# Performance work log

Measured on AMD Instinct MI355X. Metric: run time of the kernel, lower is better.

The kernel has to match this reference:

```python
import jax, jax.numpy as jnp
import numpy as np
from jax import lax

EPS = 1e-5

def _conv(x, w, pad):
    # x: NCHW, w: OIHW, stride 1
    return lax.conv_general_dilated(x, w, (1, 1), [(pad, pad), (pad, pad)],
                                    dimension_numbers=('NCHW', 'OIHW', 'NCHW'))

def _binconv(x, w):
    # IR-Net/ReActNet HardBinaryConv: sign-binarized weights scaled by per-filter
    # mean |w| (alpha), sign-binarized activations; clip-based STE for backward.
    alpha = jnp.mean(jnp.abs(w), axis=(1, 2, 3), keepdims=True)  # [O,1,1,1]
    wc = jnp.clip(w, -1.0, 1.0)
    bw = lax.stop_gradient(alpha * jnp.sign(w) - wc) + wc
    xc = jnp.clip(x, -1.0, 1.0)
    ba = lax.stop_gradient(jnp.sign(x) - xc) + xc
    return _conv(ba, bw, 1)

def _bn(x, g, b, m, v):
    # inference-mode BatchNorm2d with running stats
    inv = g / jnp.sqrt(v + EPS)
    return x * inv[None, :, None, None] + (b - m * inv)[None, :, None, None]

def _pool(x):
    return lax.reduce_window(x, -jnp.inf, lax.max, (1, 1, 2, 2), (1, 1, 2, 2), 'VALID')

def _htanh(x):
    return jnp.clip(x, -1.0, 1.0)

def setup_inputs() -> dict:
    key = jax.random.key(0)
    ks = jax.random.split(key, 40)
    B = 256
    d = {'x': jax.random.normal(ks[0], (B, 3, 32, 32), jnp.float32)}
    shapes = [(128, 3, 3, 3), (128, 128, 3, 3), (256, 128, 3, 3),
              (256, 256, 3, 3), (512, 256, 3, 3), (512, 512, 3, 3)]
    chans = [128, 128, 256, 256, 512, 512]
    ki = 1
    for i, (ws, c) in enumerate(zip(shapes, chans)):
        fan_in = ws[1] * 9
        d[f'w{i}'] = jax.random.normal(ks[ki], ws, jnp.float32) / np.sqrt(fan_in); ki += 1
        d[f'g{i}'] = jnp.ones((c,), jnp.float32)
        d[f'b{i}'] = jnp.zeros((c,), jnp.float32)
        d[f'm{i}'] = jax.random.normal(ks[ki], (c,), jnp.float32) * 0.1; ki += 1
        d[f'v{i}'] = jax.random.uniform(ks[ki], (c,), jnp.float32, 0.5, 1.5); ki += 1
    d['fcw'] = jax.random.normal(ks[ki], (10, 512 * 4 * 4), jnp.float32) * 0.01
    d['fcb'] = jnp.zeros((10,), jnp.float32)
    return d

def reference(x, w0, g0, b0, m0, v0, w1, g1, b1, m1, v1, w2, g2, b2, m2, v2,
              w3, g3, b3, m3, v3, w4, g4, b4, m4, v4, w5, g5, b5, m5, v5,
              fcw, fcb):
    h = _bn(_conv(x, w0, 1), g0, b0, m0, v0)            # [B,128,32,32]
    h = _htanh(_bn(_pool(_binconv(h, w1)), g1, b1, m1, v1))   # [B,128,16,16]
    h = _htanh(_bn(_binconv(h, w2), g2, b2, m2, v2))          # [B,256,16,16]
    h = _htanh(_bn(_pool(_binconv(h, w3)), g3, b3, m3, v3))   # [B,256,8,8]
    h = _htanh(_bn(_binconv(h, w4), g4, b4, m4, v4))          # [B,512,8,8]
    h = _htanh(_bn(_pool(_binconv(h, w5)), g5, b5, m5, v5))   # [B,512,4,4]
    h = h.reshape(h.shape[0], -1)                             # [B,8192]
    return h @ fcw.T + fcb                                    # [B,10]
```

## Files before the change

### kernel.cpp

```cpp
#include <hip/hip_runtime.h>
#include <cstdint>

#define EPS 1e-5
typedef unsigned long long u64;
typedef unsigned int u32;
typedef unsigned short u16;

struct BnArgs { const float *g[6], *b[6], *m[6], *v[6]; };
struct PackArgs { const float* w[5]; u64* wbt[5]; };

__global__ void bn_prep_all(BnArgs p, double* __restrict__ scale_all,
                            double* __restrict__ shift_all) {
    int i = blockIdx.x * 256 + threadIdx.x;
    if (i >= 1792) return;
    int l, base;
    if (i < 128)       { l = 0; base = 0; }
    else if (i < 256)  { l = 1; base = 128; }
    else if (i < 512)  { l = 2; base = 256; }
    else if (i < 768)  { l = 3; base = 512; }
    else if (i < 1280) { l = 4; base = 768; }
    else               { l = 5; base = 1280; }
    const int c = i - base;
    double inv = (double)p.g[l][c] / sqrt((double)p.v[l][c] + EPS);
    scale_all[i] = inv;
    shift_all[i] = (double)p.b[l][c] - (double)p.m[l][c] * inv;
}

__global__ void zero_out(float* __restrict__ out, int n) {
    int i = blockIdx.x * blockDim.x + threadIdx.x;
    if (i < n) out[i] = 0.f;
}

__global__ void zero_u64(u64* __restrict__ p, size_t n) {
    size_t i = (size_t)blockIdx.x * 256 + threadIdx.x;
    const size_t step = (size_t)gridDim.x * 256;
    for (; i < n; i += step) p[i] = 0ull;
}

__global__ void pack_all(PackArgs pk, const double* __restrict__ scale_all,
                         const double* __restrict__ shift_all,
                         double* __restrict__ A_all,
                         int* __restrict__ tlt_all, int* __restrict__ tgt_all,
                         u32* __restrict__ ct_all) {
    const int ob = blockIdx.x;
    const int t = threadIdx.x;
    int l, base, Cin, bnoff, OTOT, ctoff;
    if (ob < 128)       { l = 0; base = 0;    Cin = 128; bnoff = 128;  OTOT = 128; ctoff = 0; }
    else if (ob < 384)  { l = 1; base = 128;  Cin = 128; bnoff = 256;  OTOT = 256; ctoff = 2048; }
    else if (ob < 640)  { l = 2; base = 384;  Cin = 256; bnoff = 512;  OTOT = 256; ctoff = 6144; }
    else if (ob < 1152) { l = 3; base = 640;  Cin = 256; bnoff = 768;  OTOT = 512; ctoff = 10240; }
    else                { l = 4; base = 1152; Cin = 512; bnoff = 1280; OTOT = 512; ctoff = 18432; }
    const int o = ob - base;
    const float* wo = pk.w[l] + (size_t)o * Cin * 9;

    double s = 0.0;
    for (int k = t; k < Cin * 9; k += 256) s += fabs((double)wo[k]);
    __shared__ double red[256];
    __shared__ u32 stp[9];
    red[t] = s;
    if (t < 9) stp[t] = 0;
    __syncthreads();
    for (int r = 128; r > 0; r >>= 1) {
        if (t < r) red[t] += red[t + r];
        __syncthreads();
    }
    if (t == 0) {
        double alpha = red[0] / (double)(Cin * 9);
        const double dA = alpha * scale_all[bnoff + o];
        const double dB = shift_all[bnoff + o];
        A_all[ob] = dA;
        const int INF = 1 << 30;
        int Tlt, Tgt = INF;
        if (dA > 0.0) {
            const double tt = -dB / dA;
            if (!(fabs(tt) < 6000.0)) {
                Tlt = (dB < 0.0) ? INF : -INF;
            } else {
                int v0 = (int)floor(tt) - 4;
                int c = INF;
                for (int v = v0; v < v0 + 9; ++v)
                    if (fma(dA, (double)v, dB) >= 0.0) { c = v; break; }
                Tlt = c;
            }
        } else if (dA < 0.0) {
            const double tt = -dB / dA;
            if (!(fabs(tt) < 6000.0)) {
                Tlt = (dB < 0.0) ? INF : -INF;
            } else {
                int v0 = (int)floor(tt) - 4;
                int c = INF;
                for (int v = v0; v < v0 + 9; ++v)
                    if (fma(dA, (double)v, dB) < 0.0) { c = v; break; }
                Tlt = -INF;
                Tgt = (c == INF) ? INF : (c - 1);
            }
        } else {
            Tlt = (dB < 0.0) ? INF : -INF;
        }
        tlt_all[ob] = Tlt;
        tgt_all[ob] = Tgt;
    }

    const int W64 = Cin / 64;
    u64* wbt = pk.wbt[l];
    for (int e = t; e < 9 * W64; e += 256) {
        int tap = e / W64, word = e % W64;
        u64 bits = 0;
        for (int j = 0; j < 64; ++j) {
            int c = word * 64 + j;
            if (wo[c * 9 + tap] < 0.f) bits |= (1ull << j);
        }
        wbt[((size_t)tap * OTOT + o) * W64 + word] = bits;
        atomicAdd(&stp[tap], (u32)__popcll(bits));
    }
    __syncthreads();

    if (t < 16) {
        const int pat = t;
        int nv = 0;
        u32 cor = 0;
#pragma unroll
        for (int tap = 0; tap < 9; ++tap) {
            const int dy = tap / 3, dx = tap % 3;
            const bool inv = ((pat & 1) && dy == 0) || ((pat & 2) && dy == 2) ||
                             ((pat & 4) && dx == 0) || ((pat & 8) && dx == 2);
            if (inv) cor += stp[tap]; else nv++;
        }
        ct_all[ctoff + pat * OTOT + o] = (u32)(nv * 64 * W64) + 2u * cor;
    }
}

__global__ __launch_bounds__(256) void conv0_pack(
        const float* __restrict__ x, const float* __restrict__ w0,
        const double* __restrict__ scale, const double* __restrict__ shift,
        u64* __restrict__ bits0) {
    __shared__ double wlds[128 * 27];
    __shared__ double sc[128], sh[128];
    const int tid = threadIdx.x;
    for (int e = tid; e < 128 * 27; e += 256) wlds[e] = (double)w0[e];
    for (int e = tid; e < 128; e += 256) { sc[e] = scale[e]; sh[e] = shift[e]; }
    __syncthreads();

    const int n = blockIdx.y;
    const int p = blockIdx.x * 256 + tid;
    const int y = p >> 5, xx = p & 31;
    const float* xn = x + (size_t)n * 3 * 32 * 32;

    double win[27];
#pragma unroll
    for (int c = 0; c < 3; ++c)
#pragma unroll
        for (int dy = 0; dy < 3; ++dy)
#pragma unroll
            for (int dx = 0; dx < 3; ++dx) {
                const int yy = y + dy - 1, xs = xx + dx - 1;
                const bool ok = (yy >= 0 && yy < 32 && xs >= 0 && xs < 32);
                win[(c * 3 + dy) * 3 + dx] = ok ? (double)xn[(c * 32 + yy) * 32 + xs] : 0.0;
            }

    u64* op = bits0 + (((size_t)n * 34 + (y + 1)) * 34 + (xx + 1)) * 2;
#pragma unroll
    for (int og = 0; og < 2; ++og) {
        u64 word = 0;
#pragma unroll 2
        for (int j = 0; j < 64; ++j) {
            const int o = og * 64 + j;
            const double* wo = &wlds[o * 27];
            double acc = 0.0;
#pragma unroll
            for (int k = 0; k < 27; ++k) acc = fma(wo[k], win[k], acc);
            const double val = acc * sc[o] + sh[o];
            word |= (u64)(val < 0.0) << j;
        }
        op[og] = word;
    }
}

template<int H, int W, int W64, int OTOT, int OPW, bool POOL, bool LAST, int MINW>
__global__ __launch_bounds__(256, MINW) void bconv7(
        const u64* __restrict__ in_bits, const u64* __restrict__ wbt,
        const double* __restrict__ A, const double* __restrict__ B,
        const int* __restrict__ tlt, const int* __restrict__ tgt,
        const u32* __restrict__ ct_all, int ctoff,
        u32* __restrict__ out_bits, float* __restrict__ h5) {
    const int tid = threadIdx.x;
    const int wave = tid >> 6, lane = tid & 63;
    constexpr int WPI = (H * W) / 64;
    const int img = (WPI >= 4) ? blockIdx.z : (blockIdx.z * 4 + wave);
    const int wii = (WPI >= 4) ? (blockIdx.y * 4 + wave) : 0;
    const int y = wii * (64 / W) + lane / W;
    const int x = lane % W;
    const int obase = blockIdx.x * OPW;

    __shared__ u32 ctl[16 * (OPW + 1)];
    for (int e = tid; e < 16 * OPW; e += 256) {
        const int pat = e / OPW, oc = e % OPW;
        ctl[pat * (OPW + 1) + oc] = ct_all[ctoff + pat * OTOT + obase + oc];
    }
    __syncthreads();

    constexpr int RC = W + 2;
    const u64* ib = in_bits + (size_t)img * (H + 2) * RC * W64;

    int acc[OPW];
#pragma unroll
    for (int oc = 0; oc < OPW; ++oc) acc[oc] = 0;

#pragma unroll 1
    for (int dy = 0; dy < 3; ++dy) {
#pragma unroll 1
        for (int dx = 0; dx < 3; ++dx) {
            const u64* q = ib + ((size_t)(y + dy) * RC + (x + dx)) * W64;
            u64 wn[W64];
#pragma unroll
            for (int k = 0; k < W64; ++k) wn[k] = q[k];
            const u64* wt = wbt + (size_t)((dy * 3 + dx) * OTOT + obase) * W64;
#pragma unroll
            for (int oc = 0; oc < OPW; ++oc) {
#pragma unroll
                for (int k = 0; k < W64; ++k)
                    acc[oc] += (int)__popcll(wn[k] ^ wt[oc * W64 + k]);
            }
        }
    }

    const int pat = (y == 0 ? 1 : 0) | (y == H - 1 ? 2 : 0) |
                    (x == 0 ? 4 : 0) | (x == W - 1 ? 8 : 0);
    const int ctbase = pat * (OPW + 1);
    constexpr int Hp = POOL ? H / 2 : H, Wp = POOL ? W / 2 : W;
    const bool writer = (!POOL) || (((lane & 1) == 0) && ((lane & W) == 0));
    const int py = POOL ? (y >> 1) : y, px = POOL ? (x >> 1) : x;

    u32 cur = 0;
#pragma unroll
    for (int oc = 0; oc < OPW; ++oc) {
        int v = (int)ctl[ctbase + oc] - 2 * acc[oc];
        if (POOL) {
            int v2 = max(v, __shfl_xor(v, 1, 64));
            v = max(v2, __shfl_xor(v2, W, 64));
        }
        if (LAST) {
            const double t = fma(A[obase + oc], (double)v, B[obase + oc]);
            const double hcl = fmin(1.0, fmax(-1.0, t));
            if (writer)
                h5[(((size_t)img * OTOT + obase + oc) * Hp + py) * Wp + px] = (float)hcl;
        } else {
            const bool bit = (v < tlt[obase + oc]) | (v > tgt[obase + oc]);
            cur |= (u32)bit << oc;
        }
    }
    if (!LAST && writer) {
        const size_t wordIdx =
            (((size_t)img * (Hp + 2) + (py + 1)) * (Wp + 2) + (px + 1)) * (OTOT / 32)
            + (obase >> 5);
        if (OPW == 32) {
            out_bits[wordIdx] = cur;
        } else {
            u16* o16 = (u16*)out_bits;
            o16[wordIdx * 2 + ((obase >> 4) & 1)] = (u16)cur;
        }
    }
}

__global__ void fc_kernel(const float* __restrict__ h, const float* __restrict__ fcw,
                          const float* __restrict__ fcb, float* __restrict__ out) {
    const int n = blockIdx.x, t = threadIdx.x;
    double acc[10];
#pragma unroll
    for (int j = 0; j < 10; ++j) acc[j] = 0.0;
    const float* hn = h + (size_t)n * 8192;
    for (int k = t; k < 8192; k += 256) {
        double xv = (double)hn[k];
#pragma unroll
        for (int j = 0; j < 10; ++j) acc[j] += xv * (double)fcw[j * 8192 + k];
    }
    __shared__ double red[10][256];
#pragma unroll
    for (int j = 0; j < 10; ++j) red[j][t] = acc[j];
    __syncthreads();
    for (int r = 128; r > 0; r >>= 1) {
        if (t < r) {
#pragma unroll
            for (int j = 0; j < 10; ++j) red[j][t] += red[j][t + r];
        }
        __syncthreads();
    }
    if (t < 10) out[n * 10 + t] = (float)(red[t][0] + (double)fcb[t]);
}

extern "C" void kernel_launch(void* const* d_in, const int* in_sizes, int n_in,
                              void* d_out, int out_size, void* d_ws, size_t ws_size,
                              hipStream_t stream) {
    const float* X = (const float*)d_in[0];
    BnArgs bn;
    PackArgs pk;
    const float* Wt0 = (const float*)d_in[1];
    for (int i = 0; i < 6; ++i) {
        bn.g[i] = (const float*)d_in[2 + 5 * i];
        bn.b[i] = (const float*)d_in[3 + 5 * i];
        bn.m[i] = (const float*)d_in[4 + 5 * i];
        bn.v[i] = (const float*)d_in[5 + 5 * i];
    }
    for (int i = 0; i < 5; ++i) pk.w[i] = (const float*)d_in[1 + 5 * (i + 1)];
    const float* fcw = (const float*)d_in[31];
    const float* fcb = (const float*)d_in[32];
    float* out = (float*)d_out;

    char* ws = (char*)d_ws;
    size_t off = 0;
    auto alloc = [&](size_t bytes) -> void* {
        void* p = ws + off;
        off = (off + bytes + 255) & ~(size_t)255;
        return p;
    };

    double* scale_all = (double*)alloc(1792 * sizeof(double));
    double* shift_all = (double*)alloc(1792 * sizeof(double));
    double* A_all     = (double*)alloc(1664 * sizeof(double));
    int* tlt_all      = (int*)alloc(1664 * sizeof(int));
    int* tgt_all      = (int*)alloc(1664 * sizeof(int));
    u32* ct_all       = (u32*)alloc(26624 * sizeof(u32));
    const size_t WBN[5] = {128ull * 9 * 2, 256ull * 9 * 2, 256ull * 9 * 4,
                           512ull * 9 * 4, 512ull * 9 * 8};
    for (int i = 0; i < 5; ++i) pk.wbt[i] = (u64*)alloc(WBN[i] * sizeof(u64));
    u64* bits4 = (u64*)alloc(256ull * 10 * 10 * 8 * sizeof(u64));
    u64* bits0 = (u64*)alloc(256ull * 34 * 34 * 2 * sizeof(u64));
    u64* bits1 = (u64*)alloc(256ull * 18 * 18 * 2 * sizeof(u64));
    u64* bits2 = (u64*)alloc(256ull * 18 * 18 * 4 * sizeof(u64));
    u64* bits3 = (u64*)alloc(256ull * 10 * 10 * 4 * sizeof(u64));
    const size_t bits_u64 =
        256ull * (10 * 10 * 8 + 34 * 34 * 2 + 18 * 18 * 2 + 18 * 18 * 4 + 10 * 10 * 4);
    float* h5 = (float*)bits0;
    {
        const size_t h5_bytes = 256ull * 8192 * sizeof(float);
        const size_t have = (size_t)((char*)(bits3 + 256ull * 10 * 10 * 4) - (char*)bits0);
        if (h5_bytes > have) alloc(h5_bytes - have);
    }

    if (off > ws_size) {
        zero_out<<<dim3((out_size + 255) / 256), dim3(256), 0, stream>>>(out, out_size);
        return;
    }

    const int BOF[6] = {0, 128, 256, 512, 768, 1280};
    const int AOF[5] = {0, 128, 384, 640, 1152};
    const int CTO[5] = {0, 2048, 6144, 10240, 18432};

    bn_prep_all<<<dim3(7), dim3(256), 0, stream>>>(bn, scale_all, shift_all);
    pack_all<<<dim3(1664), dim3(256), 0, stream>>>(pk, scale_all, shift_all,
                                                   A_all, tlt_all, tgt_all, ct_all);
    zero_u64<<<dim3(2048), dim3(256), 0, stream>>>(bits4, bits_u64);

    conv0_pack<<<dim3(4, 256), dim3(256), 0, stream>>>(
        X, Wt0, scale_all + BOF[0], shift_all + BOF[0], bits0);

    bconv7<32, 32, 2, 128, 32, true, false, 4><<<dim3(4, 4, 256), dim3(256), 0, stream>>>(
        bits0, pk.wbt[0], nullptr, nullptr, tlt_all + AOF[0], tgt_all + AOF[0],
        ct_all, CTO[0], (u32*)bits1, nullptr);
    bconv7<16, 16, 2, 256, 32, false, false, 4><<<dim3(8, 1, 256), dim3(256), 0, stream>>>(
        bits1, pk.wbt[1], nullptr, nullptr, tlt_all + AOF[1], tgt_all + AOF[1],
        ct_all, CTO[1], (u32*)bits2, nullptr);
    bconv7<16, 16, 4, 256, 32, true, false, 4><<<dim3(8, 1, 256), dim3(256), 0, stream>>>(
        bits2, pk.wbt[2], nullptr, nullptr, tlt_all + AOF[2], tgt_all + AOF[2],
        ct_all, CTO[2], (u32*)bits3, nullptr);
    bconv7<8, 8, 4, 512, 16, false, false, 8><<<dim3(32, 1, 64), dim3(256), 0, stream>>>(
        bits3, pk.wbt[3], nullptr, nullptr, tlt_all + AOF[3], tgt_all + AOF[3],
        ct_all, CTO[3], (u32*)bits4, nullptr);
    bconv7<8, 8, 8, 512, 16, true, true, 8><<<dim3(32, 1, 64), dim3(256), 0, stream>>>(
        bits4, pk.wbt[4], A_all + AOF[4], shift_all + BOF[5], nullptr, nullptr,
        ct_all, CTO[4], nullptr, h5);

    fc_kernel<<<dim3(256), dim3(256), 0, stream>>>(h5, fcw, fcb, out);
}
```

Before: 557.7 us.

## Run last binary conv on int8 MFMA instead of XNOR-popcount kernel

```diff
diff --git a/kernel.cpp b/kernel.cpp
--- a/kernel.cpp
+++ b/kernel.cpp
@@ -5,6 +5,7 @@
 typedef unsigned long long u64;
 typedef unsigned int u32;
 typedef unsigned short u16;
+typedef int v4i __attribute__((ext_vector_type(4)));
 
 struct BnArgs { const float *g[6], *b[6], *m[6], *v[6]; };
 struct PackArgs { const float* w[5]; u64* wbt[5]; };
@@ -41,7 +42,7 @@
                          const double* __restrict__ shift_all,
                          double* __restrict__ A_all,
                          int* __restrict__ tlt_all, int* __restrict__ tgt_all,
-                         u32* __restrict__ ct_all) {
+                         u32* __restrict__ ct_all, signed char* __restrict__ wi8) {
     const int ob = blockIdx.x;
     const int t = threadIdx.x;
     int l, base, Cin, bnoff, OTOT, ctoff;
@@ -113,6 +114,13 @@
         wbt[((size_t)tap * OTOT + o) * W64 + word] = bits;
         atomicAdd(&stp[tap], (u32)__popcll(bits));
     }
+    if (l == 4) {
+        for (int e = t; e < 9 * 512; e += 256) {
+            const int tap = e / 512, c = e % 512;
+            wi8[((size_t)tap * 512 + o) * 512 + c] =
+                (wo[c * 9 + tap] < 0.f) ? (signed char)-1 : (signed char)1;
+        }
+    }
     __syncthreads();
 
     if (t < 16) {
@@ -262,6 +270,95 @@
     }
 }
 
+__global__ __launch_bounds__(256, 2) void bconv5_mfma(
+        const u64* __restrict__ bits4, const signed char* __restrict__ wi8,
+        const double* __restrict__ A, const double* __restrict__ B,
+        float* __restrict__ h5) {
+    const int tid = threadIdx.x;
+    const int wave = tid >> 6, lane = tid & 63;
+    const int img = blockIdx.y;
+    const int nhalf = blockIdx.x;
+
+    __shared__ __align__(16) signed char act[100 * 528];
+    {
+        u32* a32 = (u32*)act;
+        for (int e = tid; e < 100 * 132; e += 256) a32[e] = 0;
+        __syncthreads();
+        for (int e = tid; e < 64 * 128; e += 256) {
+            const int px = e >> 7, wi = e & 127;
+            const int cell = (px >> 3) * 10 + (px & 7) + 11;
+            const u64 bb = bits4[((size_t)img * 100 + cell) * 8 + (wi >> 4)];
+            const u32 nib = (u32)(bb >> ((wi & 15) * 4)) & 0xF;
+            const u32 spread = (nib & 1) | ((nib & 2) << 7) |
+                               ((nib & 4) << 14) | ((nib & 8) << 21);
+            a32[cell * 132 + wi] = 0x01010101u + 254u * spread;
+        }
+    }
+    __syncthreads();
+
+    const int r16 = lane & 15, kg4 = lane >> 4;
+    const int ntb = nhalf * 16 + wave * 4;
+
+    v4i acc[4][4];
+#pragma unroll
+    for (int m = 0; m < 4; ++m)
+#pragma unroll
+        for (int q = 0; q < 4; ++q) acc[m][q] = (v4i){0, 0, 0, 0};
+
+    int acell[4];
+#pragma unroll
+    for (int m = 0; m < 4; ++m) {
+        const int px = m * 16 + r16;
+        acell[m] = ((px >> 3) + (m * 2 - (px >> 3) ? 0 : 0)) * 10 + (px & 7);
+        acell[m] = (m * 2 + (r16 >> 3)) * 10 + (r16 & 7);
+    }
+
+#pragma unroll 1
+    for (int tap = 0; tap < 9; ++tap) {
+        const int coff = (tap / 3) * 10 + (tap % 3);
+        const signed char* wb = wi8 + (size_t)tap * 512 * 512;
+#pragma unroll 1
+        for (int kg = 0; kg < 8; ++kg) {
+            const int kofs = kg * 64 + kg4 * 16;
+            v4i af[4];
+#pragma unroll
+            for (int m = 0; m < 4; ++m)
+                af[m] = *(const v4i*)&act[(acell[m] + coff) * 528 + kofs];
+#pragma unroll
+            for (int q = 0; q < 4; ++q) {
+                const int oc = (ntb + q) * 16 + r16;
+                const v4i bf = *(const v4i*)&wb[(size_t)oc * 512 + kofs];
+#pragma unroll
+                for (int m = 0; m < 4; ++m)
+                    acc[m][q] = __builtin_amdgcn_mfma_i32_16x16x64_i8(
+                        af[m], bf, acc[m][q], 0, 0, 0);
+            }
+        }
+    }
+
+#pragma unroll
+    for (int m = 0; m < 4; ++m) {
+#pragma unroll
+        for (int q = 0; q < 4; ++q) {
+            const int v01 = max(acc[m][q][0], acc[m][q][1]);
+            const int v23 = max(acc[m][q][2], acc[m][q][3]);
+            const int p0 = max(v01, __shfl_xor(v01, 32, 64));
+            const int p1 = max(v23, __shfl_xor(v23, 32, 64));
+            if (kg4 < 2) {
+                const int oc = (ntb + q) * 16 + r16;
+                const int py = m;
+                const int px0 = kg4 * 2;
+                const double Av = A[oc], Bv = B[oc];
+                const double t0 = fma(Av, (double)p0, Bv);
+                const double t1 = fma(Av, (double)p1, Bv);
+                float* hp = &h5[(((size_t)img * 512 + oc) * 4 + py) * 4 + px0];
+                hp[0] = (float)fmin(1.0, fmax(-1.0, t0));
+                hp[1] = (float)fmin(1.0, fmax(-1.0, t1));
+            }
+        }
+    }
+}
+
 __global__ void fc_kernel(const float* __restrict__ h, const float* __restrict__ fcw,
                           const float* __restrict__ fcb, float* __restrict__ out) {
     const int n = blockIdx.x, t = threadIdx.x;
@@ -320,6 +417,7 @@
     int* tlt_all      = (int*)alloc(1664 * sizeof(int));
     int* tgt_all      = (int*)alloc(1664 * sizeof(int));
     u32* ct_all       = (u32*)alloc(26624 * sizeof(u32));
+    signed char* wi8  = (signed char*)alloc(9ull * 512 * 512);
     const size_t WBN[5] = {128ull * 9 * 2, 256ull * 9 * 2, 256ull * 9 * 4,
                            512ull * 9 * 4, 512ull * 9 * 8};
     for (int i = 0; i < 5; ++i) pk.wbt[i] = (u64*)alloc(WBN[i] * sizeof(u64));
@@ -348,7 +446,7 @@
 
     bn_prep_all<<<dim3(7), dim3(256), 0, stream>>>(bn, scale_all, shift_all);
     pack_all<<<dim3(1664), dim3(256), 0, stream>>>(pk, scale_all, shift_all,
-                                                   A_all, tlt_all, tgt_all, ct_all);
+                                                   A_all, tlt_all, tgt_all, ct_all, wi8);
     zero_u64<<<dim3(2048), dim3(256), 0, stream>>>(bits4, bits_u64);
 
     conv0_pack<<<dim3(4, 256), dim3(256), 0, stream>>>(
@@ -366,9 +464,9 @@
     bconv7<8, 8, 4, 512, 16, false, false, 8><<<dim3(32, 1, 64), dim3(256), 0, stream>>>(
         bits3, pk.wbt[3], nullptr, nullptr, tlt_all + AOF[3], tgt_all + AOF[3],
         ct_all, CTO[3], (u32*)bits4, nullptr);
-    bconv7<8, 8, 8, 512, 16, true, true, 8><<<dim3(32, 1, 64), dim3(256), 0, stream>>>(
-        bits4, pk.wbt[4], A_all + AOF[4], shift_all + BOF[5], nullptr, nullptr,
-        ct_all, CTO[4], nullptr, h5);
+
+    bconv5_mfma<<<dim3(2, 256), dim3(256), 0, stream>>>(
+        bits4, wi8, A_all + AOF[4], shift_all + BOF[5], h5);
 
     fc_kernel<<<dim3(256), dim3(256), 0, stream>>>(h5, fcw, fcb, out);
 }
```

Measured after the change: 574.1 us. 2.9% more time.
